# Optimization experiments

Hardware: AMD Instinct MI355X
Metric: run time of the kernel (lower is better)

The kernel has to match this reference:

```python
import jax, jax.numpy as jnp
import numpy as np

EPS_U = 1e-10
EPS_LOG = 1e-08
TEMPERATURE = 1.0


def setup_inputs() -> dict:
    key = jax.random.key(0)
    k1, k2, k3, k4 = jax.random.split(key, 4)
    B, S, D = 4, 4096, 2048
    Din = 2 * D
    scale_s = 1.0 / np.sqrt(Din)
    scale_r = 1.0 / np.sqrt(D)
    return {
        "attn1": jax.random.normal(k1, (B, S, D), dtype=jnp.float32),
        "attn2": jax.random.normal(k2, (B, S, D), dtype=jnp.float32),
        "W_share": jax.random.normal(k3, (Din, D), dtype=jnp.float32) * scale_s,
        "b_share": jnp.zeros((D,), dtype=jnp.float32),
        "W_router": jax.random.normal(k4, (D, 3), dtype=jnp.float32) * scale_r,
        "b_router": jnp.zeros((3,), dtype=jnp.float32),
    }


def gumbel_softmax_hard(logits, temperature, key):
    U = jnp.clip(jax.random.uniform(key, logits.shape, dtype=logits.dtype), EPS_U, 1.0)
    gumbels = -jnp.log(-jnp.log(U))
    y_soft = jax.nn.softmax((logits + gumbels) / temperature, axis=-1)
    index = jnp.argmax(y_soft, axis=-1)
    y_hard = jax.nn.one_hot(index, logits.shape[-1], dtype=logits.dtype)
    # straight-through estimator
    return jax.lax.stop_gradient(y_hard - y_soft) + y_soft


def reference(attn1, attn2, W_share, b_share, W_router, b_router):
    # fixed key for the gumbel noise (deterministic reference)
    noise_key = jax.random.key(42)
    combined_x = jnp.concatenate([attn1, attn2], axis=-1)        # [B,S,2D]
    x_s = combined_x @ W_share + b_share                          # [B,S,D]
    router_logits = x_s @ W_router + b_router                     # [B,S,3]
    p = gumbel_softmax_hard(router_logits, TEMPERATURE, noise_key)  # [B,S,3]
    # weighted sum of candidates (attn1, attn2, x_s) without stacking
    output = (p[..., 0:1] * attn1 + p[..., 1:2] * attn2 + p[..., 2:3] * x_s)
    entropy = -jnp.sum(p * jnp.log(p + EPS_LOG), axis=-1)         # [B,S]
    entropy_loss = -jnp.mean(entropy)
    mean_probs = p.mean(axis=(0, 1))                              # [3]
    load_balance_loss = -jnp.sum(mean_probs * jnp.log(mean_probs + EPS_LOG))
    return output, entropy_loss, load_balance_loss
```

## Files before the change

kernel.cpp:

```cpp
#include <hip/hip_runtime.h>
#include <hip/hip_fp16.h>
#include <stdint.h>

#define NROWS  16384
#define DMODEL 2048
#define DIN    4096
#define NG     (NROWS*3)

#define WS_CNT   0
#define WS_BF    256
#define WS_WF    512
#define WS_GUM   65536
#define WS_ROWL  262144
#define WS_SEGC2 327680
#define WS_SEGC1 335872
#define WS_RSEG  344064
#define WS_WH    (1u<<20)
#define WS_ACOMP (WS_WH + (16u<<20))
#define WS_ACOMP_BYTES ((size_t)NROWS * DIN * 2)

typedef __attribute__((ext_vector_type(8))) _Float16 f16x8;
typedef __attribute__((ext_vector_type(4))) float f32x4;

#define THREEFRY_PARTITIONABLE 1

__device__ __forceinline__ void tf2x32(uint32_t k0, uint32_t k1,
                                       uint32_t x0, uint32_t x1,
                                       uint32_t& o0, uint32_t& o1) {
  uint32_t k2 = k0 ^ k1 ^ 0x1BD11BDAu;
  x0 += k0; x1 += k1;
#define TFR(r) { x0 += x1; x1 = (x1 << r) | (x1 >> (32 - r)); x1 ^= x0; }
  TFR(13) TFR(15) TFR(26) TFR(6)
  x0 += k1; x1 += k2 + 1u;
  TFR(17) TFR(29) TFR(16) TFR(24)
  x0 += k2; x1 += k0 + 2u;
  TFR(13) TFR(15) TFR(26) TFR(6)
  x0 += k0; x1 += k1 + 3u;
  TFR(17) TFR(29) TFR(16) TFR(24)
  x0 += k1; x1 += k2 + 4u;
  TFR(13) TFR(15) TFR(26) TFR(6)
  x0 += k2; x1 += k0 + 5u;
#undef TFR
  o0 = x0; o1 = x1;
}

__global__ __launch_bounds__(1024)
void k_init(int* __restrict__ cnt, int* __restrict__ segz) {
  const int t = threadIdx.x;
  if (t < 8) cnt[t] = 0;
#pragma unroll
  for (int i = 0; i < 4; ++i) segz[t + (i << 10)] = 0;
}

__global__ void k_gumbel(float* __restrict__ g) {
  int j = blockIdx.x * blockDim.x + threadIdx.x;
  if (j >= NG) return;
  uint32_t b0, b1, bits;
#if THREEFRY_PARTITIONABLE
  tf2x32(0u, 42u, 0u, (uint32_t)j, b0, b1);
  bits = b0 ^ b1;
#else
  const int half = NG / 2;
  if (j < half) { tf2x32(0u, 42u, (uint32_t)j, (uint32_t)(j + half), b0, b1); bits = b0; }
  else          { tf2x32(0u, 42u, (uint32_t)(j - half), (uint32_t)j, b0, b1); bits = b1; }
#endif
  float U = __uint_as_float((bits >> 9) | 0x3f800000u) - 1.0f;
  U = fmaxf(U, 1e-10f);
  U = fminf(U, 1.0f);
  g[j] = -logf(-logf(U));
}

__global__ __launch_bounds__(256)
void k_wfused(const float* __restrict__ Ws, const float* __restrict__ bsh,
              const float* __restrict__ Wr, const float* __restrict__ br,
              float* __restrict__ Wf, float* __restrict__ bf) {
  const int k = blockIdx.x;
  const int t = threadIdx.x;
  const float* src = (k < DIN) ? (Ws + (size_t)k * DMODEL) : bsh;
  float4 x0 = *(const float4*)(src + t * 8);
  float4 x1 = *(const float4*)(src + t * 8 + 4);
  float xv[8] = {x0.x, x0.y, x0.z, x0.w, x1.x, x1.y, x1.z, x1.w};
  float4 w4[6];
  const float4* wp = (const float4*)(Wr + t * 24);
#pragma unroll
  for (int i = 0; i < 6; ++i) w4[i] = wp[i];
  const float* wfv = (const float*)w4;
  float z0 = 0.f, z1 = 0.f, z2 = 0.f;
#pragma unroll
  for (int jj = 0; jj < 8; ++jj) {
    z0 = fmaf(xv[jj], wfv[jj*3+0], z0);
    z1 = fmaf(xv[jj], wfv[jj*3+1], z1);
    z2 = fmaf(xv[jj], wfv[jj*3+2], z2);
  }
#pragma unroll
  for (int off = 32; off > 0; off >>= 1) {
    z0 += __shfl_down(z0, off, 64);
    z1 += __shfl_down(z1, off, 64);
    z2 += __shfl_down(z2, off, 64);
  }
  __shared__ float red[4][3];
  int lane = t & 63, wv = t >> 6;
  if (lane == 0) { red[wv][0] = z0; red[wv][1] = z1; red[wv][2] = z2; }
  __syncthreads();
  if (t == 0) {
    float s0 = red[0][0] + red[1][0] + red[2][0] + red[3][0];
    float s1 = red[0][1] + red[1][1] + red[2][1] + red[3][1];
    float s2 = red[0][2] + red[1][2] + red[2][2] + red[3][2];
    if (k < DIN) { Wf[k] = s0; Wf[4096 + k] = s1; Wf[8192 + k] = s2; }
    else { bf[0] = s0 + br[0]; bf[1] = s1 + br[1]; bf[2] = s2 + br[2]; }
  }
}

__device__ __forceinline__ uint16_t f16b(float x) {
  return __half_as_ushort(__float2half(x));
}
__device__ __forceinline__ uint2 pack4h(float4 v) {
  return make_uint2((uint32_t)f16b(v.x) | ((uint32_t)f16b(v.y) << 16),
                    (uint32_t)f16b(v.z) | ((uint32_t)f16b(v.w) << 16));
}

__global__ __launch_bounds__(256)
void k_wsplit(const float* __restrict__ Ws, uint16_t* __restrict__ Wh) {
  const int kt = blockIdx.x;
  const int nb = blockIdx.y;
  const int k0 = kt << 6, n0 = nb << 6;
  __shared__ float T[64][65];
  const int t = threadIdx.x;
#pragma unroll
  for (int r = 0; r < 4; ++r) {
    int lin = r * 256 + t;
    int ki = lin >> 4;
    int nj = (lin & 15) << 2;
    float4 v = *(const float4*)(Ws + (size_t)(k0 + ki) * DMODEL + n0 + nj);
    T[ki][nj+0] = v.x; T[ki][nj+1] = v.y; T[ki][nj+2] = v.z; T[ki][nj+3] = v.w;
  }
  __syncthreads();
#pragma unroll
  for (int r = 0; r < 4; ++r) {
    int lin = r * 256 + t;
    int nl = lin >> 4;
    int k4 = (lin & 15) << 2;
    int ng = n0 + nl;
    int c = k4 >> 3, e0 = k4 & 7;
    float x0 = T[k4+0][nl], x1 = T[k4+1][nl], x2 = T[k4+2][nl], x3 = T[k4+3][nl];
    size_t off = ((size_t)ng << 12) + k0 + ((size_t)((c ^ (ng & 7)) << 3)) + e0;
    *(uint2*)(Wh + off) = make_uint2((uint32_t)f16b(x0) | ((uint32_t)f16b(x1) << 16),
                                     (uint32_t)f16b(x2) | ((uint32_t)f16b(x3) << 16));
  }
}

__global__ __launch_bounds__(256)
void k_router(const float* __restrict__ a1, const float* __restrict__ a2,
              const float* __restrict__ Wf, const float* __restrict__ bf,
              const float* __restrict__ gum, float* __restrict__ out,
              int* __restrict__ segc1, int* __restrict__ segc2,
              int* __restrict__ rowl_seg) {
  const int t = threadIdx.x;
  const int lane = t & 63, w = t >> 6;
  const int row = (int)blockIdx.x * 4 + w;
  const float* pa = a1 + ((size_t)row << 11) + (lane << 2);
  const float* pb = a2 + ((size_t)row << 11) + (lane << 2);
  const float* w0 = Wf + (lane << 2);
  const float* w1 = Wf + 4096 + (lane << 2);
  const float* w2 = Wf + 8192 + (lane << 2);
  float z0 = 0.f, z1 = 0.f, z2 = 0.f;
#pragma unroll
  for (int c = 0; c < 8; ++c) {
    const int k = c << 8;
    float4 a = *(const float4*)(pa + k);
    float4 u0 = *(const float4*)(w0 + k);
    float4 u1 = *(const float4*)(w1 + k);
    float4 u2 = *(const float4*)(w2 + k);
    z0 = fmaf(a.x,u0.x,fmaf(a.y,u0.y,fmaf(a.z,u0.z,fmaf(a.w,u0.w,z0))));
    z1 = fmaf(a.x,u1.x,fmaf(a.y,u1.y,fmaf(a.z,u1.z,fmaf(a.w,u1.w,z1))));
    z2 = fmaf(a.x,u2.x,fmaf(a.y,u2.y,fmaf(a.z,u2.z,fmaf(a.w,u2.w,z2))));
    float4 b = *(const float4*)(pb + k);
    float4 v0 = *(const float4*)(w0 + 2048 + k);
    float4 v1 = *(const float4*)(w1 + 2048 + k);
    float4 v2 = *(const float4*)(w2 + 2048 + k);
    z0 = fmaf(b.x,v0.x,fmaf(b.y,v0.y,fmaf(b.z,v0.z,fmaf(b.w,v0.w,z0))));
    z1 = fmaf(b.x,v1.x,fmaf(b.y,v1.y,fmaf(b.z,v1.z,fmaf(b.w,v1.w,z1))));
    z2 = fmaf(b.x,v2.x,fmaf(b.y,v2.y,fmaf(b.z,v2.z,fmaf(b.w,v2.w,z2))));
  }
#pragma unroll
  for (int m = 1; m < 64; m <<= 1) {
    z0 += __shfl_xor(z0, m, 64);
    z1 += __shfl_xor(z1, m, 64);
    z2 += __shfl_xor(z2, m, 64);
  }
  const float l0 = z0 + bf[0] + gum[row*3+0];
  const float l1 = z1 + bf[1] + gum[row*3+1];
  const float l2 = z2 + bf[2] + gum[row*3+2];
  int idx = 0; float m = l0;
  if (l1 > m) { m = l1; idx = 1; }
  if (l2 > m) { idx = 2; }

  if (lane == 0) {
    const int seg = row >> 8;
    if (idx == 1) {
      atomicAdd(segc1 + (seg << 5), 1);
    } else if (idx == 2) {
      int p = atomicAdd(segc2 + (seg << 5), 1);
      rowl_seg[(seg << 8) + p] = row;
    }
  }
  if (idx < 2) {
    const float* src = (idx == 0) ? pa : pb;
    float* po = out + ((size_t)row << 11) + (lane << 2);
#pragma unroll
    for (int c = 0; c < 8; ++c)
      *(float4*)(po + (c << 8)) = *(const float4*)(src + (c << 8));
  }
}

__global__ __launch_bounds__(256)
void k_fixup(const int* __restrict__ segc1, const int* __restrict__ segc2,
             const int* __restrict__ rowl_seg, int* __restrict__ cnt,
             int* __restrict__ rowl) {
  __shared__ int scnt[64], sstart[64];
  const int t = threadIdx.x;
  if (t < 64) scnt[t] = segc2[t << 5];
  __syncthreads();
  if (t == 0) {
    int acc = 0, s1 = 0;
#pragma unroll
    for (int g = 0; g < 64; ++g) { sstart[g] = acc; acc += scnt[g]; }
#pragma unroll
    for (int g = 0; g < 64; ++g) s1 += segc1[g << 5];
    cnt[2] = acc; cnt[1] = s1; cnt[0] = NROWS - acc - s1;
  }
  __syncthreads();
  for (int g = 0; g < 64; ++g) {
    int c = scnt[g], base = sstart[g];
    for (int i = t; i < c; i += 256) rowl[base + i] = rowl_seg[(g << 8) + i];
  }
}

__global__ __launch_bounds__(256)
void k_acomp(const float* __restrict__ a1, const float* __restrict__ a2,
             const int* __restrict__ cnt, const int* __restrict__ rowl,
             uint16_t* __restrict__ acomp) {
  const int t = threadIdx.x;
  const int lane = t & 63, w = t >> 6;
  const int i = (int)blockIdx.x * 4 + w;
  if (i >= cnt[2]) return;
  const int row = rowl[i];
  const int psw = i & 7;
  uint16_t* ar = acomp + ((size_t)i << 12);
  const float* pa = a1 + ((size_t)row << 11);
  const float* pb = a2 + ((size_t)row << 11);
#pragma unroll
  for (int it = 0; it < 8; ++it) {
    int e = (it << 8) + (lane << 2);
    float4 va = *(const float4*)(pa + e);
    float4 vb = *(const float4*)(pb + e);
    int g = e >> 6, c = (e >> 3) & 7, o = e & 7;
    int d = (g << 6) + ((c ^ psw) << 3) + o;
    *(uint2*)(ar + d) = pack4h(va);
    *(uint2*)(ar + 2048 + d) = pack4h(vb);
  }
}

template<int AMODE>
__global__ __launch_bounds__(256, 4)
void k_gemm_fp16(const float* __restrict__ a1, const float* __restrict__ a2,
                 const uint16_t* __restrict__ Acomp,
                 const uint16_t* __restrict__ Wh,
                 const float* __restrict__ bsh, const int* __restrict__ cnt,
                 const int* __restrict__ rowl, float* __restrict__ out) {
  const int M = cnt[2];
  const int nwg = (int)gridDim.x;
  const int mTiles = nwg >> 4;
  int xcd = blockIdx.x & 7, rest = blockIdx.x >> 3;
  int q = nwg >> 3, r = nwg & 7;
  int swz = (xcd < r ? xcd * (q + 1) : r * (q + 1) + (xcd - r) * q) + rest;
  const int bm = swz % mTiles;
  const int bn = swz / mTiles;
  if (bm * 128 >= M) return;
  const int n0 = bn << 7;

  __shared__ uint16_t AS[128 * 64];
  __shared__ uint16_t BhS[128 * 64];
  __shared__ int rows[128];
  const int t = threadIdx.x;
  const int lane = t & 63, w = t >> 6;
  const int wm = w >> 1, wn = w & 1;
  if (t < 128) { int i = bm * 128 + t; rows[t] = (i < M) ? rowl[i] : -1; }
  __syncthreads();

  f32x4 acc[4][4];
#pragma unroll
  for (int fm = 0; fm < 4; ++fm)
#pragma unroll
    for (int fn = 0; fn < 4; ++fn) acc[fm][fn] = (f32x4){0.f, 0.f, 0.f, 0.f};
  float bias[4];
#pragma unroll
  for (int fn = 0; fn < 4; ++fn)
    bias[fn] = bsh[n0 + (wn << 6) + (fn << 4) + (lane & 15)];

  const size_t arow0 = ((size_t)(bm << 7)) << 12;

  for (int kt = 0; kt < 64; ++kt) {
    __syncthreads();
#pragma unroll
    for (int i = 0; i < 4; ++i) {
      int idx = (w << 8) + (i << 6) + lane;
      int nrow = idx >> 3, c = idx & 7;
      size_t goff = ((size_t)(n0 + nrow) << 12) + (kt << 6) + (c << 3);
      __builtin_amdgcn_global_load_lds(
          (const __attribute__((address_space(1))) void*)(Wh + goff),
          (__attribute__((address_space(3))) void*)((char*)BhS + (w << 12) + (i << 10)),
          16, 0, 0);
    }
    if (AMODE == 0) {
#pragma unroll
      for (int i = 0; i < 4; ++i) {
        int idx = (w << 8) + (i << 6) + lane;
        int m = idx >> 3, c = idx & 7;
        const uint16_t* src = Acomp + arow0 + (((size_t)m) << 12) + (kt << 6) + (c << 3);
        __builtin_amdgcn_global_load_lds(
            (const __attribute__((address_space(1))) void*)src,
            (__attribute__((address_space(3))) void*)((char*)AS + (w << 12) + (i << 10)),
            16, 0, 0);
      }
    } else {
#pragma unroll
      for (int i = 0; i < 4; ++i) {
        int idx = t + (i << 8);
        int m = idx >> 3, c = idx & 7;
        int row = rows[m];
        float4 v0 = make_float4(0.f,0.f,0.f,0.f), v1 = v0;
        if (row >= 0) {
          const float* s = (kt < 32)
              ? (a1 + (size_t)row * DMODEL + (kt << 6) + (c << 3))
              : (a2 + (size_t)row * DMODEL + ((kt - 32) << 6) + (c << 3));
          v0 = *(const float4*)s; v1 = *(const float4*)(s + 4);
        }
        uint32_t q0 = (uint32_t)f16b(v0.x) | ((uint32_t)f16b(v0.y) << 16);
        uint32_t q1 = (uint32_t)f16b(v0.z) | ((uint32_t)f16b(v0.w) << 16);
        uint32_t q2 = (uint32_t)f16b(v1.x) | ((uint32_t)f16b(v1.y) << 16);
        uint32_t q3 = (uint32_t)f16b(v1.z) | ((uint32_t)f16b(v1.w) << 16);
        *(uint4*)((char*)AS + m * 128 + ((c ^ (m & 7)) << 4)) = make_uint4(q0, q1, q2, q3);
      }
    }
    __syncthreads();
#pragma unroll
    for (int ks = 0; ks < 2; ++ks) {
      const int chb = (ks << 2) | (lane >> 4);
      f16x8 af[4];
#pragma unroll
      for (int fm = 0; fm < 4; ++fm) {
        int rm = (wm << 6) + (fm << 4) + (lane & 15);
        af[fm] = *(const f16x8*)((const char*)AS + rm * 128 + ((chb ^ (rm & 7)) << 4));
      }
#pragma unroll
      for (int fn = 0; fn < 4; ++fn) {
        int rn = (wn << 6) + (fn << 4) + (lane & 15);
        int sw = (chb ^ (rn & 7)) << 4;
        f16x8 bh = *(const f16x8*)((const char*)BhS + rn * 128 + sw);
#pragma unroll
        for (int fm = 0; fm < 4; ++fm)
          acc[fm][fn] = __builtin_amdgcn_mfma_f32_16x16x32_f16(af[fm], bh, acc[fm][fn], 0, 0, 0);
      }
    }
  }
#pragma unroll
  for (int fm = 0; fm < 4; ++fm) {
    int rbase = (wm << 6) + (fm << 4) + ((lane >> 4) << 2);
#pragma unroll
    for (int j = 0; j < 4; ++j) {
      int row = rows[rbase + j];
      if (row < 0) continue;
      float* po = out + (size_t)row * DMODEL + n0 + (wn << 6) + (lane & 15);
#pragma unroll
      for (int fn = 0; fn < 4; ++fn)
        po[fn << 4] = acc[fm][fn][j] + bias[fn];
    }
  }
}

#define BM 128
#define BN 128
#define BK 32
__global__ __launch_bounds__(256)
void k_gemm_f32(const float* __restrict__ a1, const float* __restrict__ a2,
                const float* __restrict__ Ws, const float* __restrict__ bsh,
                const int* __restrict__ cnt, const int* __restrict__ rowl,
                float* __restrict__ out) {
  const int M = cnt[2];
  const int bm = blockIdx.x;
  if (bm * BM >= M) return;
  const int bn = blockIdx.y;
  __shared__ float As[BK][132];
  __shared__ float Bs[BK][128];
  __shared__ int rows[BM];
  const int t = threadIdx.x;
  if (t < BM) {
    int i = bm * BM + t;
    rows[t] = (i < M) ? rowl[i] : -1;
  }
  __syncthreads();
  float acc[8][8];
#pragma unroll
  for (int i = 0; i < 8; ++i)
#pragma unroll
    for (int j = 0; j < 8; ++j) acc[i][j] = 0.f;
  const int tx = t & 15, ty = t >> 4;
  for (int k0 = 0; k0 < DIN; k0 += BK) {
    const float* Abase = (k0 < DMODEL) ? a1 : a2;
    const int kb = (k0 < DMODEL) ? k0 : (k0 - DMODEL);
    float4 av[4], bv4[4];
#pragma unroll
    for (int r = 0; r < 4; ++r) {
      int lin = r * 256 + t;
      int mi = lin >> 3;
      int ki = (lin & 7) << 2;
      int row = rows[mi];
      av[r] = (row >= 0) ? *(const float4*)(Abase + (size_t)row * DMODEL + kb + ki)
                         : make_float4(0.f, 0.f, 0.f, 0.f);
    }
#pragma unroll
    for (int r = 0; r < 4; ++r) {
      int lin = r * 256 + t;
      int ki = lin >> 5;
      int ni = (lin & 31) << 2;
      bv4[r] = *(const float4*)(Ws + (size_t)(k0 + ki) * DMODEL + bn * BN + ni);
    }
    __syncthreads();
#pragma unroll
    for (int r = 0; r < 4; ++r) {
      int lin = r * 256 + t;
      int mi = lin >> 3;
      int ki = (lin & 7) << 2;
      As[ki + 0][mi] = av[r].x;
      As[ki + 1][mi] = av[r].y;
      As[ki + 2][mi] = av[r].z;
      As[ki + 3][mi] = av[r].w;
      int k2 = lin >> 5;
      int ni = (lin & 31) << 2;
      *(float4*)(&Bs[k2][ni]) = bv4[r];
    }
    __syncthreads();
#pragma unroll
    for (int kk = 0; kk < BK; ++kk) {
      float4 aL = *(const float4*)(&As[kk][ty << 2]);
      float4 aH = *(const float4*)(&As[kk][64 + (ty << 2)]);
      float4 bL = *(const float4*)(&Bs[kk][tx << 2]);
      float4 bH = *(const float4*)(&Bs[kk][64 + (tx << 2)]);
      float am[8] = {aL.x, aL.y, aL.z, aL.w, aH.x, aH.y, aH.z, aH.w};
      float bb[8] = {bL.x, bL.y, bL.z, bL.w, bH.x, bH.y, bH.z, bH.w};
#pragma unroll
      for (int i = 0; i < 8; ++i)
#pragma unroll
        for (int j = 0; j < 8; ++j)
          acc[i][j] = fmaf(am[i], bb[j], acc[i][j]);
    }
  }
  float bias[8];
#pragma unroll
  for (int j = 0; j < 4; ++j) {
    bias[j]     = bsh[bn * BN + (tx << 2) + j];
    bias[4 + j] = bsh[bn * BN + 64 + (tx << 2) + j];
  }
#pragma unroll
  for (int i = 0; i < 8; ++i) {
    int m = (i < 4) ? ((ty << 2) + i) : (64 + (ty << 2) + (i - 4));
    int row = rows[m];
    if (row < 0) continue;
    float* po = out + (size_t)row * DMODEL + bn * BN;
    float4 v0 = make_float4(acc[i][0] + bias[0], acc[i][1] + bias[1],
                            acc[i][2] + bias[2], acc[i][3] + bias[3]);
    float4 v1 = make_float4(acc[i][4] + bias[4], acc[i][5] + bias[5],
                            acc[i][6] + bias[6], acc[i][7] + bias[7]);
    *(float4*)(po + (tx << 2)) = v0;
    *(float4*)(po + 64 + (tx << 2)) = v1;
  }
}

__global__ void k_loss(const int* __restrict__ cnt, float* __restrict__ o) {
  if (threadIdx.x == 0 && blockIdx.x == 0) {
    const float inv = 1.0f / (float)NROWS;
    float lb = 0.f;
#pragma unroll
    for (int e = 0; e < 3; ++e) {
      float m = (float)cnt[e] * inv;
      lb -= m * logf(m + 1e-8f);
    }
    o[0] = 0.0f;
    o[1] = lb;
  }
}

extern "C" void kernel_launch(void* const* d_in, const int* in_sizes, int n_in,
                              void* d_out, int out_size, void* d_ws, size_t ws_size,
                              hipStream_t stream) {
  const float* a1  = (const float*)d_in[0];
  const float* a2  = (const float*)d_in[1];
  const float* Ws  = (const float*)d_in[2];
  const float* bsh = (const float*)d_in[3];
  const float* Wr  = (const float*)d_in[4];
  const float* br  = (const float*)d_in[5];
  float* out = (float*)d_out;
  char* ws = (char*)d_ws;
  int*      cnt   = (int*)(ws + WS_CNT);
  float*    bf    = (float*)(ws + WS_BF);
  float*    Wf    = (float*)(ws + WS_WF);
  float*    gum   = (float*)(ws + WS_GUM);
  int*      rowl  = (int*)(ws + WS_ROWL);
  int*      segc2 = (int*)(ws + WS_SEGC2);
  int*      segc1 = (int*)(ws + WS_SEGC1);
  int*      rseg  = (int*)(ws + WS_RSEG);
  uint16_t* Wh    = (uint16_t*)(ws + WS_WH);
  uint16_t* Acomp = (uint16_t*)(ws + WS_ACOMP);
  float* losses = out + (size_t)NROWS * DMODEL;

  const bool fp16path = ws_size >= (size_t)WS_ACOMP;
  const bool fullA = ws_size >= (size_t)WS_ACOMP + WS_ACOMP_BYTES;

  hipLaunchKernelGGL(k_init,   dim3(1),              dim3(1024), 0, stream, cnt, segc2);
  hipLaunchKernelGGL(k_gumbel, dim3((NG + 255)/256), dim3(256), 0, stream, gum);
  hipLaunchKernelGGL(k_wfused, dim3(DIN + 1),        dim3(256), 0, stream, Ws, bsh, Wr, br, Wf, bf);
  if (fp16path) {
    hipLaunchKernelGGL(k_wsplit, dim3(64, 32),       dim3(256), 0, stream, Ws, Wh);
    hipLaunchKernelGGL(k_router, dim3(NROWS / 4),    dim3(256), 0, stream,
                       a1, a2, Wf, bf, gum, out, segc1, segc2, rseg);
    hipLaunchKernelGGL(k_fixup,  dim3(1),            dim3(256), 0, stream,
                       segc1, segc2, rseg, cnt, rowl);
    if (fullA) {
      hipLaunchKernelGGL(k_acomp, dim3(NROWS / 4),   dim3(256), 0, stream,
                         a1, a2, cnt, rowl, Acomp);
      hipLaunchKernelGGL((k_gemm_fp16<0>), dim3((NROWS / 128) * 16), dim3(256), 0, stream,
                         a1, a2, Acomp, Wh, bsh, cnt, rowl, out);
    } else {
      hipLaunchKernelGGL((k_gemm_fp16<1>), dim3((NROWS / 128) * 16), dim3(256), 0, stream,
                         a1, a2, Acomp, Wh, bsh, cnt, rowl, out);
    }
  } else {
    hipLaunchKernelGGL(k_router, dim3(NROWS / 4),    dim3(256), 0, stream,
                       a1, a2, Wf, bf, gum, out, segc1, segc2, rseg);
    hipLaunchKernelGGL(k_fixup,  dim3(1),            dim3(256), 0, stream,
                       segc1, segc2, rseg, cnt, rowl);
    hipLaunchKernelGGL(k_gemm_f32, dim3(NROWS / BM, DMODEL / BN), dim3(256), 0, stream,
                       a1, a2, Ws, bsh, cnt, rowl, out);
  }
  hipLaunchKernelGGL(k_loss,   dim3(1),              dim3(64),  0, stream, cnt, losses);
}
```

Before: 300.7 us.

## Halve GEMM N-tile to 64, raise occupancy, fold init and loss kernels

The fp16 GEMM now uses 128x64 tiles instead of 128x128. That doubles the grid, halves the B shared-memory buffer and the accumulators, and raises the launch_bounds occupancy hint to 6. The goal is to fill the GPU better when only a fraction of rows (M = cnt[2]) are routed to the GEMM. The counter zeroing moves into the gumbel kernel and the load-balance loss moves into k_fixup, which removes two tiny kernel launches. The cost is more A-tile reloads, since each A tile is read by twice as many workgroups, and lower arithmetic intensity per workgroup.

```diff
diff --git a/kernel.cpp b/kernel.cpp
--- a/kernel.cpp
+++ b/kernel.cpp
@@ -44,16 +44,17 @@
   o0 = x0; o1 = x1;
 }
 
-__global__ __launch_bounds__(1024)
-void k_init(int* __restrict__ cnt, int* __restrict__ segz) {
-  const int t = threadIdx.x;
-  if (t < 8) cnt[t] = 0;
-#pragma unroll
-  for (int i = 0; i < 4; ++i) segz[t + (i << 10)] = 0;
-}
-
-__global__ void k_gumbel(float* __restrict__ g) {
-  int j = blockIdx.x * blockDim.x + threadIdx.x;
+__global__ void k_gumbel(float* __restrict__ g, int* __restrict__ cnt,
+                         int* __restrict__ segz) {
+  const int t = threadIdx.x;
+  if (blockIdx.x < 4) {
+    int base = ((int)blockIdx.x << 10) + (t << 2);
+#pragma unroll
+    for (int i = 0; i < 4; ++i) segz[base + i] = 0;
+  } else if (blockIdx.x == 4 && t < 8) {
+    cnt[t] = 0;
+  }
+  int j = blockIdx.x * blockDim.x + t;
   if (j >= NG) return;
   uint32_t b0, b1, bits;
 #if THREEFRY_PARTITIONABLE
@@ -216,7 +217,7 @@
 __global__ __launch_bounds__(256)
 void k_fixup(const int* __restrict__ segc1, const int* __restrict__ segc2,
              const int* __restrict__ rowl_seg, int* __restrict__ cnt,
-             int* __restrict__ rowl) {
+             int* __restrict__ rowl, float* __restrict__ losses) {
   __shared__ int scnt[64], sstart[64];
   const int t = threadIdx.x;
   if (t < 64) scnt[t] = segc2[t << 5];
@@ -228,6 +229,14 @@
 #pragma unroll
     for (int g = 0; g < 64; ++g) s1 += segc1[g << 5];
     cnt[2] = acc; cnt[1] = s1; cnt[0] = NROWS - acc - s1;
+    const float inv = 1.0f / (float)NROWS;
+    float m0 = (float)(NROWS - acc - s1) * inv;
+    float m1 = (float)s1 * inv;
+    float m2 = (float)acc * inv;
+    float lb = -(m0 * logf(m0 + 1e-8f) + m1 * logf(m1 + 1e-8f)
+               + m2 * logf(m2 + 1e-8f));
+    losses[0] = 0.0f;
+    losses[1] = lb;
   }
   __syncthreads();
   for (int g = 0; g < 64; ++g) {
@@ -262,7 +271,7 @@
 }
 
 template<int AMODE>
-__global__ __launch_bounds__(256, 4)
+__global__ __launch_bounds__(256, 6)
 void k_gemm_fp16(const float* __restrict__ a1, const float* __restrict__ a2,
                  const uint16_t* __restrict__ Acomp,
                  const uint16_t* __restrict__ Wh,
@@ -270,17 +279,17 @@
                  const int* __restrict__ rowl, float* __restrict__ out) {
   const int M = cnt[2];
   const int nwg = (int)gridDim.x;
-  const int mTiles = nwg >> 4;
+  const int mTiles = nwg >> 5;
   int xcd = blockIdx.x & 7, rest = blockIdx.x >> 3;
   int q = nwg >> 3, r = nwg & 7;
   int swz = (xcd < r ? xcd * (q + 1) : r * (q + 1) + (xcd - r) * q) + rest;
   const int bm = swz % mTiles;
   const int bn = swz / mTiles;
   if (bm * 128 >= M) return;
-  const int n0 = bn << 7;
+  const int n0 = bn << 6;
 
   __shared__ uint16_t AS[128 * 64];
-  __shared__ uint16_t BhS[128 * 64];
+  __shared__ uint16_t BhS[64 * 64];
   __shared__ int rows[128];
   const int t = threadIdx.x;
   const int lane = t & 63, w = t >> 6;
@@ -288,28 +297,28 @@
   if (t < 128) { int i = bm * 128 + t; rows[t] = (i < M) ? rowl[i] : -1; }
   __syncthreads();
 
-  f32x4 acc[4][4];
+  f32x4 acc[4][2];
 #pragma unroll
   for (int fm = 0; fm < 4; ++fm)
 #pragma unroll
-    for (int fn = 0; fn < 4; ++fn) acc[fm][fn] = (f32x4){0.f, 0.f, 0.f, 0.f};
-  float bias[4];
-#pragma unroll
-  for (int fn = 0; fn < 4; ++fn)
-    bias[fn] = bsh[n0 + (wn << 6) + (fn << 4) + (lane & 15)];
+    for (int fn = 0; fn < 2; ++fn) acc[fm][fn] = (f32x4){0.f, 0.f, 0.f, 0.f};
+  float bias[2];
+#pragma unroll
+  for (int fn = 0; fn < 2; ++fn)
+    bias[fn] = bsh[n0 + (wn << 5) + (fn << 4) + (lane & 15)];
 
   const size_t arow0 = ((size_t)(bm << 7)) << 12;
 
   for (int kt = 0; kt < 64; ++kt) {
     __syncthreads();
 #pragma unroll
-    for (int i = 0; i < 4; ++i) {
-      int idx = (w << 8) + (i << 6) + lane;
+    for (int i = 0; i < 2; ++i) {
+      int idx = (w << 7) + (i << 6) + lane;
       int nrow = idx >> 3, c = idx & 7;
       size_t goff = ((size_t)(n0 + nrow) << 12) + (kt << 6) + (c << 3);
       __builtin_amdgcn_global_load_lds(
           (const __attribute__((address_space(1))) void*)(Wh + goff),
-          (__attribute__((address_space(3))) void*)((char*)BhS + (w << 12) + (i << 10)),
+          (__attribute__((address_space(3))) void*)((char*)BhS + (w << 11) + (i << 10)),
           16, 0, 0);
     }
     if (AMODE == 0) {
@@ -354,8 +363,8 @@
         af[fm] = *(const f16x8*)((const char*)AS + rm * 128 + ((chb ^ (rm & 7)) << 4));
       }
 #pragma unroll
-      for (int fn = 0; fn < 4; ++fn) {
-        int rn = (wn << 6) + (fn << 4) + (lane & 15);
+      for (int fn = 0; fn < 2; ++fn) {
+        int rn = (wn << 5) + (fn << 4) + (lane & 15);
         int sw = (chb ^ (rn & 7)) << 4;
         f16x8 bh = *(const f16x8*)((const char*)BhS + rn * 128 + sw);
 #pragma unroll
@@ -371,9 +380,9 @@
     for (int j = 0; j < 4; ++j) {
       int row = rows[rbase + j];
       if (row < 0) continue;
-      float* po = out + (size_t)row * DMODEL + n0 + (wn << 6) + (lane & 15);
-#pragma unroll
-      for (int fn = 0; fn < 4; ++fn)
+      float* po = out + (size_t)row * DMODEL + n0 + (wn << 5) + (lane & 15);
+#pragma unroll
+      for (int fn = 0; fn < 2; ++fn)
         po[fn << 4] = acc[fm][fn][j] + bias[fn];
     }
   }
@@ -474,20 +483,6 @@
                             acc[i][6] + bias[6], acc[i][7] + bias[7]);
     *(float4*)(po + (tx << 2)) = v0;
     *(float4*)(po + 64 + (tx << 2)) = v1;
-  }
-}
-
-__global__ void k_loss(const int* __restrict__ cnt, float* __restrict__ o) {
-  if (threadIdx.x == 0 && blockIdx.x == 0) {
-    const float inv = 1.0f / (float)NROWS;
-    float lb = 0.f;
-#pragma unroll
-    for (int e = 0; e < 3; ++e) {
-      float m = (float)cnt[e] * inv;
-      lb -= m * logf(m + 1e-8f);
-    }
-    o[0] = 0.0f;
-    o[1] = lb;
   }
 }
 
@@ -517,31 +512,29 @@
   const bool fp16path = ws_size >= (size_t)WS_ACOMP;
   const bool fullA = ws_size >= (size_t)WS_ACOMP + WS_ACOMP_BYTES;
 
-  hipLaunchKernelGGL(k_init,   dim3(1),              dim3(1024), 0, stream, cnt, segc2);
-  hipLaunchKernelGGL(k_gumbel, dim3((NG + 255)/256), dim3(256), 0, stream, gum);
+  hipLaunchKernelGGL(k_gumbel, dim3((NG + 255)/256), dim3(256), 0, stream, gum, cnt, segc2);
   hipLaunchKernelGGL(k_wfused, dim3(DIN + 1),        dim3(256), 0, stream, Ws, bsh, Wr, br, Wf, bf);
   if (fp16path) {
     hipLaunchKernelGGL(k_wsplit, dim3(64, 32),       dim3(256), 0, stream, Ws, Wh);
     hipLaunchKernelGGL(k_router, dim3(NROWS / 4),    dim3(256), 0, stream,
                        a1, a2, Wf, bf, gum, out, segc1, segc2, rseg);
     hipLaunchKernelGGL(k_fixup,  dim3(1),            dim3(256), 0, stream,
-                       segc1, segc2, rseg, cnt, rowl);
+                       segc1, segc2, rseg, cnt, rowl, losses);
     if (fullA) {
       hipLaunchKernelGGL(k_acomp, dim3(NROWS / 4),   dim3(256), 0, stream,
                          a1, a2, cnt, rowl, Acomp);
-      hipLaunchKernelGGL((k_gemm_fp16<0>), dim3((NROWS / 128) * 16), dim3(256), 0, stream,
+      hipLaunchKernelGGL((k_gemm_fp16<0>), dim3((NROWS / 128) * 32), dim3(256), 0, stream,
                          a1, a2, Acomp, Wh, bsh, cnt, rowl, out);
     } else {
-      hipLaunchKernelGGL((k_gemm_fp16<1>), dim3((NROWS / 128) * 16), dim3(256), 0, stream,
+      hipLaunchKernelGGL((k_gemm_fp16<1>), dim3((NROWS / 128) * 32), dim3(256), 0, stream,
                          a1, a2, Acomp, Wh, bsh, cnt, rowl, out);
     }
   } else {
     hipLaunchKernelGGL(k_router, dim3(NROWS / 4),    dim3(256), 0, stream,
                        a1, a2, Wf, bf, gum, out, segc1, segc2, rseg);
     hipLaunchKernelGGL(k_fixup,  dim3(1),            dim3(256), 0, stream,
-                       segc1, segc2, rseg, cnt, rowl);
+                       segc1, segc2, rseg, cnt, rowl, losses);
     hipLaunchKernelGGL(k_gemm_f32, dim3(NROWS / BM, DMODEL / BN), dim3(256), 0, stream,
                        a1, a2, Ws, bsh, cnt, rowl, out);
   }
-  hipLaunchKernelGGL(k_loss,   dim3(1),              dim3(64),  0, stream, cnt, losses);
-}
+}
```

After: 364.4 us. 21.2% more time.
